# Kernel tuning notes

Measured on AMD Instinct MI355X. Metric: run time of the kernel, lower is better.

## Reference

```python
import jax, jax.numpy as jnp
import numpy as np

N = 40000        # num nodes
E = 640000       # num edges
F_IN = 512
F_OUT = 32
HEADS = 8
NEG_SLOPE = 0.2
EPS = 1e-16


def setup_inputs() -> dict:
    key = jax.random.key(0)
    k1, k2, k3, k4, k5 = jax.random.split(key, 5)
    x = jax.random.normal(k1, (N, F_IN), dtype=jnp.float32)
    edge_index = jax.random.randint(k2, (2, E), 0, N, dtype=jnp.int32)
    # xavier-uniform-like init scales
    lim_W = float(np.sqrt(6.0 / (F_IN + F_OUT)))
    lim_a = float(np.sqrt(6.0 / (HEADS + F_OUT)))
    W = jax.random.uniform(k3, (HEADS, F_IN, F_OUT), dtype=jnp.float32, minval=-lim_W, maxval=lim_W)
    a_src = jax.random.uniform(k4, (HEADS, F_OUT), dtype=jnp.float32, minval=-lim_a, maxval=lim_a)
    a_dst = jax.random.uniform(k5, (HEADS, F_OUT), dtype=jnp.float32, minval=-lim_a, maxval=lim_a)
    bias = jnp.zeros((HEADS * F_OUT,), dtype=jnp.float32)
    return {"x": x, "edge_index": edge_index, "W": W, "a_src": a_src, "a_dst": a_dst, "bias": bias}


def reference(x, edge_index, W, a_src, a_dst, bias):
    src, dst = edge_index[0], edge_index[1]
    # per-head projection: [N, H, F_out]
    h = jnp.einsum('nd,hdf->nhf', x, W)
    # attention logit pieces computed per-node then gathered per-edge
    # (same math as gathering h then dotting with a)
    s_src = jnp.einsum('nhf,hf->nh', h, a_src)   # [N, H]
    s_dst = jnp.einsum('nhf,hf->nh', h, a_dst)   # [N, H]
    e = s_src[src] + s_dst[dst]                  # [E, H]
    e = jnp.where(e >= 0, e, NEG_SLOPE * e)      # LeakyReLU(0.2)
    # edge softmax over incoming edges of each dst node (global max shift, as in source)
    e = e - jnp.max(e)
    exp_e = jnp.exp(e)
    denom = jax.ops.segment_sum(exp_e, dst, num_segments=N)   # [N, H]
    alpha = exp_e / (denom[dst] + EPS)                        # [E, H]
    # weighted message aggregation (dropout is identity in eval / p=0)
    msg = alpha[..., None] * h[src]                           # [E, H, F_out]
    out = jax.ops.segment_sum(msg, dst, num_segments=N)       # [N, H, F_out]
    out = out.reshape(N, HEADS * F_OUT) + bias                # concat=True
    return out
```

## Files before the change

kernel.cpp:

```cpp
#include <hip/hip_runtime.h>
#include <hip/hip_bf16.h>
#include <math.h>
#include <stdint.h>

#define N_NODES 40000
#define N_EDGES 640000
#define F_IN    512
#define F_OUT   32
#define HEADS   8
#define C_OUT   (HEADS * F_OUT)
#define NEG_SLOPE 0.2f
#define EPS_F   1e-16f

typedef __attribute__((ext_vector_type(8)))  short  short8;
typedef __attribute__((ext_vector_type(4)))  short  short4v;
typedef __attribute__((ext_vector_type(16))) float  float16v;

__device__ __forceinline__ void splitT(float f, unsigned short& hi, unsigned short& lo) {
    unsigned u = __float_as_uint(f);
    hi = (unsigned short)(u >> 16);
    float r = f - __uint_as_float(u & 0xFFFF0000u);
    lo = (unsigned short)(__float_as_uint(r) >> 16);
}

__device__ __forceinline__ unsigned short f2bf(float f) {
    unsigned u = __float_as_uint(f);
    return (unsigned short)((u + 0x7FFF + ((u >> 16) & 1)) >> 16);
}

__global__ __launch_bounds__(256) void pack_and_count(const float* __restrict__ W,
                                                      unsigned short* __restrict__ Bp,
                                                      const int* __restrict__ dst,
                                                      int* __restrict__ count) {
    if (blockIdx.x < 512) {
        int tid = blockIdx.x * 256 + threadIdx.x;
        int j    = tid & 7;
        int L    = (tid >> 3) & 63;
        int ni   = (tid >> 9) & 1;
        int ktg  = (tid >> 10) & 31;
        int wc   = tid >> 15;
        int k    = ktg * 16 + (L >> 5) * 8 + j;
        int col  = wc * 64 + ni * 32 + (L & 31);
        int hh = col >> 5, f = col & 31;
        Bp[tid] = f2bf(W[hh * (F_IN * F_OUT) + k * F_OUT + f]);
    } else {
        int e = (blockIdx.x - 512) * 256 + threadIdx.x;
        atomicAdd(&count[dst[e]], 1);
    }
}

#define AS 66

__global__ __launch_bounds__(256, 4) void gemm_mfma(const float* __restrict__ x,
                                                    const unsigned short* __restrict__ Bp,
                                                    const float* __restrict__ a_src,
                                                    const float* __restrict__ a_dst,
                                                    unsigned short* __restrict__ h16,
                                                    float* __restrict__ s_src,
                                                    float* __restrict__ s_dst) {
    __shared__ unsigned short As_hi[2][32 * AS];
    __shared__ unsigned short As_lo[2][32 * AS];

    const int t = threadIdx.x;
    const int wc = t >> 6, L = t & 63;
    const int r31 = L & 31, half = L >> 5;
    const int n0 = blockIdx.x * 32;

    float16v acc[2];
#pragma unroll
    for (int ni = 0; ni < 2; ++ni)
#pragma unroll
        for (int r = 0; r < 16; ++r) acc[ni][r] = 0.f;

    const int kcol = (t & 15) * 4;
    const int rbase = t >> 4;
    const float* xr0 = &x[(size_t)(n0 + rbase) * F_IN + kcol];
    const float* xr1 = &x[(size_t)(n0 + rbase + 16) * F_IN + kcol];

#define CONVW(b, s0, s1) do {                                                  \
        unsigned short h0,h1,h2,h3,l0,l1,l2,l3;                                \
        splitT((s0).x,h0,l0); splitT((s0).y,h1,l1);                            \
        splitT((s0).z,h2,l2); splitT((s0).w,h3,l3);                            \
        *(short4v*)&As_hi[b][rbase*AS + kcol] =                                \
            (short4v){(short)h0,(short)h1,(short)h2,(short)h3};                \
        *(short4v*)&As_lo[b][rbase*AS + kcol] =                                \
            (short4v){(short)l0,(short)l1,(short)l2,(short)l3};                \
        splitT((s1).x,h0,l0); splitT((s1).y,h1,l1);                            \
        splitT((s1).z,h2,l2); splitT((s1).w,h3,l3);                            \
        *(short4v*)&As_hi[b][(rbase+16)*AS + kcol] =                           \
            (short4v){(short)h0,(short)h1,(short)h2,(short)h3};                \
        *(short4v*)&As_lo[b][(rbase+16)*AS + kcol] =                           \
            (short4v){(short)l0,(short)l1,(short)l2,(short)l3};                \
    } while (0)

    float4 stg[2][2];
    stg[0][0] = *(const float4*)(xr0);
    stg[0][1] = *(const float4*)(xr1);
    CONVW(0, stg[0][0], stg[0][1]);
    stg[1][0] = *(const float4*)(xr0 + 64);
    stg[1][1] = *(const float4*)(xr1 + 64);

#pragma unroll
    for (int st = 0; st < 8; ++st) {
        const int cur = st & 1, nxt = cur ^ 1;
        __syncthreads();

        short8 breg[4][2];
#pragma unroll
        for (int kt = 0; kt < 4; ++kt)
#pragma unroll
            for (int ni = 0; ni < 2; ++ni) {
                size_t idx = ((((size_t)wc * 32 + (st * 4 + kt)) * 2 + ni) * 64 + L) * 8;
                breg[kt][ni] = *(const short8*)&Bp[idx];
            }

        if (st < 6) {
            stg[cur][0] = *(const float4*)(xr0 + (st + 2) * 64);
            stg[cur][1] = *(const float4*)(xr1 + (st + 2) * 64);
        }

#pragma unroll
        for (int kt = 0; kt < 4; ++kt) {
            int off = r31 * AS + kt * 16 + half * 8;
            short8 ah = *(const short8*)&As_hi[cur][off];
            short8 al = *(const short8*)&As_lo[cur][off];
#pragma unroll
            for (int ni = 0; ni < 2; ++ni) {
                acc[ni] = __builtin_amdgcn_mfma_f32_32x32x16_bf16(ah, breg[kt][ni], acc[ni], 0, 0, 0);
                acc[ni] = __builtin_amdgcn_mfma_f32_32x32x16_bf16(al, breg[kt][ni], acc[ni], 0, 0, 0);
            }
        }

        if (st < 7) CONVW(nxt, stg[nxt][0], stg[nxt][1]);
    }
#undef CONVW

#pragma unroll
    for (int ni = 0; ni < 2; ++ni) {
        int colb = wc * 64 + ni * 32 + r31;
#pragma unroll
        for (int r = 0; r < 16; ++r) {
            int row = n0 + (r & 3) + 8 * (r >> 2) + 4 * half;
            h16[(size_t)row * C_OUT + colb] = f2bf(acc[ni][r]);
        }
    }

#pragma unroll
    for (int ni = 0; ni < 2; ++ni) {
        int hh = wc * 2 + ni;
        float af = a_src[hh * 32 + r31];
        float df = a_dst[hh * 32 + r31];
#pragma unroll
        for (int r = 0; r < 16; ++r) {
            float v = acc[ni][r];
            float vs = v * af;
            float vd = v * df;
#pragma unroll
            for (int m = 1; m < 32; m <<= 1) {
                vs += __shfl_xor(vs, m, 64);
                vd += __shfl_xor(vd, m, 64);
            }
            if (r31 == 0) {
                int row = n0 + (r & 3) + 8 * (r >> 2) + 4 * half;
                s_src[row * 8 + hh] = vs;
                s_dst[row * 8 + hh] = vd;
            }
        }
    }
}

__global__ __launch_bounds__(1024) void scan_local(const int* __restrict__ count,
                                                   int* __restrict__ row_excl,
                                                   int* __restrict__ cursor,
                                                   int* __restrict__ btot) {
    __shared__ int woff[16];
    __shared__ int tot_s;
    const int b = blockIdx.x, t = threadIdx.x;
    const int lane = t & 63, wid = t >> 6;
    const int i = b * 1000 + t;
    int v = (t < 1000) ? count[i] : 0;
    int inc = v;
#pragma unroll
    for (int d = 1; d < 64; d <<= 1) {
        int u = __shfl_up(inc, d, 64);
        if (lane >= d) inc += u;
    }
    if (lane == 63) woff[wid] = inc;
    __syncthreads();
    if (t < 16) {
        int s = woff[t];
        int sc = s;
#pragma unroll
        for (int d = 1; d < 16; d <<= 1) {
            int u = __shfl_up(sc, d, 64);
            if (t >= d) sc += u;
        }
        woff[t] = sc - s;
        if (t == 15) tot_s = sc;
    }
    __syncthreads();
    int excl = woff[wid] + inc - v;
    if (t < 1000) { row_excl[i] = excl; cursor[i] = excl; }
    if (t == 0) btot[b] = tot_s;
}

__global__ __launch_bounds__(64) void scan_tots(const int* __restrict__ btot,
                                                int* __restrict__ boff) {
    const int t = threadIdx.x;
    int v = (t < 40) ? btot[t] : 0;
    int inc = v;
#pragma unroll
    for (int d = 1; d < 64; d <<= 1) {
        int u = __shfl_up(inc, d, 64);
        if (t >= d) inc += u;
    }
    if (t < 40) boff[t] = inc - v;
}

__global__ __launch_bounds__(256) void scatter_edges(const int* __restrict__ src,
                                                     const int* __restrict__ dst,
                                                     int* __restrict__ cursor,
                                                     const int* __restrict__ boff,
                                                     int* __restrict__ src_sorted) {
    int e = blockIdx.x * 256 + threadIdx.x;
    int s = src[e], d = dst[e];
    int pos = atomicAdd(&cursor[d], 1) + boff[d / 1000];
    src_sorted[pos] = s;
}

__global__ __launch_bounds__(256) void aggregate(const int* __restrict__ src_sorted,
                                                 const unsigned short* __restrict__ h16,
                                                 const float* __restrict__ s_src,
                                                 const float* __restrict__ s_dst,
                                                 const int* __restrict__ row_excl,
                                                 const int* __restrict__ boff,
                                                 const int* __restrict__ count,
                                                 const float* __restrict__ bias,
                                                 float* __restrict__ out) {
    const int t = threadIdx.x;
    const int wave = t >> 6, lane = t & 63;
    const int wgid = blockIdx.x * 4 + wave;
    const int ch0 = lane * 4;
    const int hh = lane >> 3;

    auto bf2f = [](short v) { return __uint_as_float(((unsigned)(unsigned short)v) << 16); };
    const float4 b4 = *(const float4*)&bias[ch0];

    for (int n = wgid; n < N_NODES; n += 8192) {
        const int start = row_excl[n] + boff[n / 1000];
        const int cnt = count[n];
        const float sd = s_dst[n * 8 + hh];

        float a0 = 0.f, a1 = 0.f, a2 = 0.f, a3 = 0.f, den = 0.f;

        int base = 0;
        for (; base + 8 <= cnt; base += 8) {
            int idx = start + base;
            int s[8];
#pragma unroll
            for (int u = 0; u < 8; ++u)
                s[u] = src_sorted[idx + u];

            short4v v[8];
#pragma unroll
            for (int u = 0; u < 8; ++u)
                v[u] = *(const short4v*)&h16[(size_t)s[u] * C_OUT + ch0];

            float w[8];
#pragma unroll
            for (int u = 0; u < 8; ++u) {
                float e = s_src[s[u] * 8 + hh] + sd;
                e = e >= 0.f ? e : NEG_SLOPE * e;
                w[u] = __expf(e);
            }

#pragma unroll
            for (int u = 0; u < 8; ++u) {
                a0 += w[u] * bf2f(v[u][0]);
                a1 += w[u] * bf2f(v[u][1]);
                a2 += w[u] * bf2f(v[u][2]);
                a3 += w[u] * bf2f(v[u][3]);
                den += w[u];
            }
        }

        int rem = cnt - base;
        if (rem > 0) {
            int idx = start + base;
            int s[8];
#pragma unroll
            for (int u = 0; u < 8; ++u)
                s[u] = (u < rem) ? src_sorted[idx + u] : 0;

            short4v v[8];
#pragma unroll
            for (int u = 0; u < 8; ++u)
                v[u] = *(const short4v*)&h16[(size_t)s[u] * C_OUT + ch0];

            float w[8];
#pragma unroll
            for (int u = 0; u < 8; ++u) {
                float e = s_src[s[u] * 8 + hh] + sd;
                e = e >= 0.f ? e : NEG_SLOPE * e;
                w[u] = (u < rem) ? __expf(e) : 0.f;
            }

#pragma unroll
            for (int u = 0; u < 8; ++u) {
                a0 += w[u] * bf2f(v[u][0]);
                a1 += w[u] * bf2f(v[u][1]);
                a2 += w[u] * bf2f(v[u][2]);
                a3 += w[u] * bf2f(v[u][3]);
                den += w[u];
            }
        }

        float inv = 1.0f / (den + EPS_F);
        float4 o;
        o.x = a0 * inv + b4.x;
        o.y = a1 * inv + b4.y;
        o.z = a2 * inv + b4.z;
        o.w = a3 * inv + b4.w;
        *(float4*)&out[(size_t)n * C_OUT + ch0] = o;
    }
}

extern "C" void kernel_launch(void* const* d_in, const int* in_sizes, int n_in,
                              void* d_out, int out_size, void* d_ws, size_t ws_size,
                              hipStream_t stream) {
    const float* x     = (const float*)d_in[0];
    const int*   eidx  = (const int*)d_in[1];
    const float* W     = (const float*)d_in[2];
    const float* a_src = (const float*)d_in[3];
    const float* a_dst = (const float*)d_in[4];
    const float* bias  = (const float*)d_in[5];
    float* out = (float*)d_out;

    const int* src = eidx;
    const int* dst = eidx + N_EDGES;

    char* p = (char*)d_ws;
    auto carve = [&](size_t bytes) {
        char* r = p;
        p += (bytes + 255) & ~(size_t)255;
        return r;
    };
    unsigned short* h16 = (unsigned short*)carve((size_t)N_NODES * C_OUT * 2);
    float* s_src      = (float*)carve((size_t)N_NODES * HEADS * 4);
    float* s_dst      = (float*)carve((size_t)N_NODES * HEADS * 4);
    int*   src_sorted = (int*)carve((size_t)N_EDGES * 4);
    int*   count      = (int*)carve((size_t)N_NODES * 4);
    int*   row_excl   = (int*)carve((size_t)N_NODES * 4);
    int*   cursor     = (int*)carve((size_t)N_NODES * 4);
    int*   btot       = (int*)carve(64 * 4);
    int*   boff       = (int*)carve(64 * 4);
    unsigned short* Bp = (unsigned short*)carve((size_t)131072 * 2);

    hipMemsetAsync(count, 0, (size_t)N_NODES * 4, stream);

    pack_and_count<<<512 + N_EDGES / 256, 256, 0, stream>>>(W, Bp, dst, count);
    gemm_mfma<<<1250, 256, 0, stream>>>(x, Bp, a_src, a_dst, h16, s_src, s_dst);
    scan_local<<<40, 1024, 0, stream>>>(count, row_excl, cursor, btot);
    scan_tots<<<1, 64, 0, stream>>>(btot, boff);
    scatter_edges<<<N_EDGES / 256, 256, 0, stream>>>(src, dst, cursor, boff, src_sorted);
    aggregate<<<2048, 256, 0, stream>>>(src_sorted, h16, s_src, s_dst,
                                        row_excl, boff, count, bias, out);
}
```

Measured before the change: 298.0 us.

## Load x fragments directly into registers, removing LDS staging in GEMM

The GEMM kernel stops staging x tiles through double-buffered shared memory. Each lane now loads its own MFMA A-fragment straight from global memory and splits it into bf16 hi/lo in registers, with a one-step register prefetch of both x and B fragments. This drops the LDS writes and reads and all __syncthreads barriers. In exchange, each of the four waves independently reloads and reconverts the same x rows (4x redundant global loads and split work), and the per-lane loads are less coalesced.

```diff
diff --git a/kernel.cpp b/kernel.cpp
--- a/kernel.cpp
+++ b/kernel.cpp
@@ -49,8 +49,6 @@
     }
 }
 
-#define AS 66
-
 __global__ __launch_bounds__(256, 4) void gemm_mfma(const float* __restrict__ x,
                                                     const unsigned short* __restrict__ Bp,
                                                     const float* __restrict__ a_src,
@@ -58,9 +56,6 @@
                                                     unsigned short* __restrict__ h16,
                                                     float* __restrict__ s_src,
                                                     float* __restrict__ s_dst) {
-    __shared__ unsigned short As_hi[2][32 * AS];
-    __shared__ unsigned short As_lo[2][32 * AS];
-
     const int t = threadIdx.x;
     const int wc = t >> 6, L = t & 63;
     const int r31 = L & 31, half = L >> 5;
@@ -72,68 +67,43 @@
 #pragma unroll
         for (int r = 0; r < 16; ++r) acc[ni][r] = 0.f;
 
-    const int kcol = (t & 15) * 4;
-    const int rbase = t >> 4;
-    const float* xr0 = &x[(size_t)(n0 + rbase) * F_IN + kcol];
-    const float* xr1 = &x[(size_t)(n0 + rbase + 16) * F_IN + kcol];
-
-#define CONVW(b, s0, s1) do {                                                  \
-        unsigned short h0,h1,h2,h3,l0,l1,l2,l3;                                \
-        splitT((s0).x,h0,l0); splitT((s0).y,h1,l1);                            \
-        splitT((s0).z,h2,l2); splitT((s0).w,h3,l3);                            \
-        *(short4v*)&As_hi[b][rbase*AS + kcol] =                                \
-            (short4v){(short)h0,(short)h1,(short)h2,(short)h3};                \
-        *(short4v*)&As_lo[b][rbase*AS + kcol] =                                \
-            (short4v){(short)l0,(short)l1,(short)l2,(short)l3};                \
-        splitT((s1).x,h0,l0); splitT((s1).y,h1,l1);                            \
-        splitT((s1).z,h2,l2); splitT((s1).w,h3,l3);                            \
-        *(short4v*)&As_hi[b][(rbase+16)*AS + kcol] =                           \
-            (short4v){(short)h0,(short)h1,(short)h2,(short)h3};                \
-        *(short4v*)&As_lo[b][(rbase+16)*AS + kcol] =                           \
-            (short4v){(short)l0,(short)l1,(short)l2,(short)l3};                \
-    } while (0)
-
-    float4 stg[2][2];
-    stg[0][0] = *(const float4*)(xr0);
-    stg[0][1] = *(const float4*)(xr1);
-    CONVW(0, stg[0][0], stg[0][1]);
-    stg[1][0] = *(const float4*)(xr0 + 64);
-    stg[1][1] = *(const float4*)(xr1 + 64);
-
-#pragma unroll
-    for (int st = 0; st < 8; ++st) {
-        const int cur = st & 1, nxt = cur ^ 1;
-        __syncthreads();
-
-        short8 breg[4][2];
-#pragma unroll
-        for (int kt = 0; kt < 4; ++kt)
-#pragma unroll
-            for (int ni = 0; ni < 2; ++ni) {
-                size_t idx = ((((size_t)wc * 32 + (st * 4 + kt)) * 2 + ni) * 64 + L) * 8;
-                breg[kt][ni] = *(const short8*)&Bp[idx];
-            }
-
-        if (st < 6) {
-            stg[cur][0] = *(const float4*)(xr0 + (st + 2) * 64);
-            stg[cur][1] = *(const float4*)(xr1 + (st + 2) * 64);
-        }
-
-#pragma unroll
-        for (int kt = 0; kt < 4; ++kt) {
-            int off = r31 * AS + kt * 16 + half * 8;
-            short8 ah = *(const short8*)&As_hi[cur][off];
-            short8 al = *(const short8*)&As_lo[cur][off];
-#pragma unroll
-            for (int ni = 0; ni < 2; ++ni) {
-                acc[ni] = __builtin_amdgcn_mfma_f32_32x32x16_bf16(ah, breg[kt][ni], acc[ni], 0, 0, 0);
-                acc[ni] = __builtin_amdgcn_mfma_f32_32x32x16_bf16(al, breg[kt][ni], acc[ni], 0, 0, 0);
-            }
-        }
-
-        if (st < 7) CONVW(nxt, stg[nxt][0], stg[nxt][1]);
-    }
-#undef CONVW
+    const float* xp = &x[(size_t)(n0 + r31) * F_IN + half * 8];
+    const unsigned short* bp = &Bp[((size_t)wc * 32 * 2 * 64 + L) * 8];
+
+    float4 nxa = *(const float4*)(xp);
+    float4 nxb = *(const float4*)(xp + 4);
+    short8 nb0 = *(const short8*)(bp);
+    short8 nb1 = *(const short8*)(bp + 512);
+
+#pragma unroll
+    for (int kt = 0; kt < 32; ++kt) {
+        float4 xa = nxa, xb = nxb;
+        short8 c0 = nb0, c1 = nb1;
+        if (kt < 31) {
+            nxa = *(const float4*)(xp + (kt + 1) * 16);
+            nxb = *(const float4*)(xp + (kt + 1) * 16 + 4);
+            nb0 = *(const short8*)(bp + (size_t)(kt + 1) * 1024);
+            nb1 = *(const short8*)(bp + (size_t)(kt + 1) * 1024 + 512);
+        }
+
+        short8 ah, al;
+        {
+            unsigned short h, l;
+            splitT(xa.x, h, l); ah[0] = (short)h; al[0] = (short)l;
+            splitT(xa.y, h, l); ah[1] = (short)h; al[1] = (short)l;
+            splitT(xa.z, h, l); ah[2] = (short)h; al[2] = (short)l;
+            splitT(xa.w, h, l); ah[3] = (short)h; al[3] = (short)l;
+            splitT(xb.x, h, l); ah[4] = (short)h; al[4] = (short)l;
+            splitT(xb.y, h, l); ah[5] = (short)h; al[5] = (short)l;
+            splitT(xb.z, h, l); ah[6] = (short)h; al[6] = (short)l;
+            splitT(xb.w, h, l); ah[7] = (short)h; al[7] = (short)l;
+        }
+
+        acc[0] = __builtin_amdgcn_mfma_f32_32x32x16_bf16(ah, c0, acc[0], 0, 0, 0);
+        acc[1] = __builtin_amdgcn_mfma_f32_32x32x16_bf16(ah, c1, acc[1], 0, 0, 0);
+        acc[0] = __builtin_amdgcn_mfma_f32_32x32x16_bf16(al, c0, acc[0], 0, 0, 0);
+        acc[1] = __builtin_amdgcn_mfma_f32_32x32x16_bf16(al, c1, acc[1], 0, 0, 0);
+    }
 
 #pragma unroll
     for (int ni = 0; ni < 2; ++ni) {
```

Result: slower. 325.9 us (+9.4%).
